# Kernel tuning notes

Hardware: AMD Instinct MI355X
Metric: run time of the kernel (lower is better)

Reference implementation:

```python
import jax, jax.numpy as jnp
import numpy as np

B, M, K = 8, 2048, 64          # clouds, points per cloud, max neighbors
C_IN, C_OUT, R = 64, 64, 0.2   # channels, radius
BN_EPS = 1e-5                  # BatchNorm eval: running_mean=0, running_var=1


def _bn(y, g, b):
    # eval-mode BatchNorm1d with running stats (0, 1)
    return g * y * (1.0 / jnp.sqrt(1.0 + BN_EPS)) + b


def _lin_init(key, fan_in, shape):
    s = 1.0 / np.sqrt(fan_in)
    return jax.random.uniform(key, shape, jnp.float32, -s, s)


def setup_inputs() -> dict:
    key = jax.random.key(0)
    ks = jax.random.split(key, 16)
    N = B * M
    pos = jax.random.uniform(ks[0], (N, 3), jnp.float32)
    x = jax.random.normal(ks[1], (N, C_IN), jnp.float32)
    nrm = jax.random.normal(ks[2], (N, 3), jnp.float32)
    normal = nrm / jnp.linalg.norm(nrm, axis=-1, keepdims=True)
    batch = jnp.repeat(jnp.arange(B, dtype=jnp.int32), M)
    return {
        "x": x, "pos": pos, "normal": normal, "batch": batch,
        # PointTransformerConv linear layers (value / key / query)
        "lin_w": _lin_init(ks[3], C_IN, (C_IN, C_OUT)),
        "lin_b": _lin_init(ks[4], C_IN, (C_OUT,)),
        "lin_src_w": _lin_init(ks[5], C_IN, (C_IN, C_OUT)),
        "lin_src_b": _lin_init(ks[6], C_IN, (C_OUT,)),
        "lin_dst_w": _lin_init(ks[7], C_IN, (C_IN, C_OUT)),
        "lin_dst_b": _lin_init(ks[8], C_IN, (C_OUT,)),
        # pos_nn = MLP([6, C_OUT]): Linear -> BN -> ReLU (Dropout off in eval)
        "pos_w": _lin_init(ks[9], 6, (6, C_OUT)),
        "pos_b": _lin_init(ks[10], 6, (C_OUT,)),
        "pos_g": jnp.ones((C_OUT,), jnp.float32),
        "pos_bt": jnp.zeros((C_OUT,), jnp.float32),
        # attn_nn = MLP([C_OUT, C_OUT])
        "attn_w": _lin_init(ks[11], C_OUT, (C_OUT, C_OUT)),
        "attn_b": _lin_init(ks[12], C_OUT, (C_OUT,)),
        "attn_g": jnp.ones((C_OUT,), jnp.float32),
        "attn_bt": jnp.zeros((C_OUT,), jnp.float32),
    }


def _forward(x, pos, normal, lin_w, lin_b, lin_src_w, lin_src_b,
             lin_dst_w, lin_dst_b, pos_w, pos_b, pos_g, pos_bt,
             attn_w, attn_b, attn_g, attn_bt):
    xb = x.reshape(B, M, C_IN)
    pb = pos.reshape(B, M, 3)
    nb = normal.reshape(B, M, 3)

    # radius(pos, pos, r, batch, batch, max_num_neighbors=K):
    # per-cloud pairwise sq-distances -> K nearest, masked to d <= r.
    d2 = jnp.sum((pb[:, :, None, :] - pb[:, None, :, :]) ** 2, axis=-1)  # [B,M,M]
    neg_d2, idx = jax.lax.top_k(-d2, K)                                   # [B,M,K]
    mask = (-neg_d2) <= R * R                                             # self always valid

    gather = jax.vmap(lambda a, i: a[i])  # per-cloud gather: [M,C],[M,K] -> [M,K,C]

    v = xb @ lin_w + lin_b          # value   [B,M,C]
    kf = xb @ lin_src_w + lin_src_b # key     [B,M,C]
    q = xb @ lin_dst_w + lin_dst_b  # query   [B,M,C]

    vj = gather(v, idx)             # [B,M,K,C]
    kj = gather(kf, idx)
    pj = gather(pb, idx)            # [B,M,K,3]
    nj = gather(nb, idx)

    rel = jnp.concatenate([pb[:, :, None, :] - pj,
                           nb[:, :, None, :] - nj], axis=-1)  # [B,M,K,6]
    delta = jax.nn.relu(_bn(rel @ pos_w + pos_b, pos_g, pos_bt))  # [B,M,K,C]

    alpha = jax.nn.relu(_bn((q[:, :, None, :] - kj + delta) @ attn_w + attn_b,
                            attn_g, attn_bt))                     # [B,M,K,C]
    alpha = jnp.where(mask[..., None], alpha, -jnp.inf)
    w = jax.nn.softmax(alpha, axis=2)                              # softmax over neighbors

    out = jnp.sum(w * (vj + delta), axis=2)                        # [B,M,C]
    return out.reshape(B * M, C_OUT)


def reference(x, pos, normal, batch, lin_w, lin_b, lin_src_w, lin_src_b,
              lin_dst_w, lin_dst_b, pos_w, pos_b, pos_g, pos_bt,
              attn_w, attn_b, attn_g, attn_bt):
    del batch  # batch ids are block-contiguous: encoded by the [B,M] reshape
    return _forward(x, pos, normal, lin_w, lin_b, lin_src_w, lin_src_b,
                    lin_dst_w, lin_dst_b, pos_w, pos_b, pos_g, pos_bt,
                    attn_w, attn_b, attn_g, attn_bt)
```

## Files before the change

kernel.cpp:

```cpp
#include <hip/hip_runtime.h>
#include <math.h>

#define BB 8
#define MM 2048
#define NTOT (BB*MM)
#define R2 0.04f
#define CAP 256

typedef _Float16 h8 __attribute__((ext_vector_type(8)));
typedef _Float16 h4 __attribute__((ext_vector_type(4)));
typedef float f32x4 __attribute__((ext_vector_type(4)));

__device__ __forceinline__ int swz(int row, int col) {
  return (row << 6) + ((((col >> 3) ^ (row & 7)) << 3) | (col & 7));
}

__device__ __forceinline__ unsigned long long shfl_xor_u64(unsigned long long x, int off) {
  int lo = __shfl_xor((int)(unsigned)(x & 0xFFFFFFFFull), off, 64);
  int hi = __shfl_xor((int)(unsigned)(x >> 32), off, 64);
  return (((unsigned long long)(unsigned)hi) << 32) | (unsigned)lo;
}
__device__ __forceinline__ unsigned long long wave_min_u64(unsigned long long x) {
#pragma unroll
  for (int off = 32; off; off >>= 1) {
    unsigned long long o = shfl_xor_u64(x, off);
    x = (o < x) ? o : x;
  }
  return x;
}
__device__ __forceinline__ unsigned long long wave_max_u64(unsigned long long x) {
#pragma unroll
  for (int off = 32; off; off >>= 1) {
    unsigned long long o = shfl_xor_u64(x, off);
    x = (o > x) ? o : x;
  }
  return x;
}

__global__ __launch_bounds__(256) void prep_w(
    const float* __restrict__ attn_w, const float* __restrict__ pos_w,
    const float* __restrict__ lin_w, const float* __restrict__ lsw, const float* __restrict__ ldw,
    const float* __restrict__ lsb, const float* __restrict__ ldb,
    const float* __restrict__ pos_b, const float* __restrict__ pos_g, const float* __restrict__ pos_bt,
    const float* __restrict__ attn_b, const float* __restrict__ attn_g, const float* __restrict__ attn_bt,
    unsigned short* __restrict__ w_img, unsigned short* __restrict__ pw_img,
    unsigned short* __restrict__ pj_img, float* __restrict__ bnc) {
  __shared__ float sWa[4096];
  __shared__ float sK[256], sQ[256];
  const int tid = threadIdx.x, blk = blockIdx.x;
  for (int i = tid; i < 4096; i += 256) sWa[i] = attn_w[i];
  {
    const int r = tid >> 6, c = tid & 63;
    sK[tid] = lsw[(blk * 4 + r) * 64 + c];
    sQ[tid] = ldw[(blk * 4 + r) * 64 + c];
  }
  __syncthreads();
  const int idx = blk * 256 + tid;
  const int d = idx >> 6, cc = idx & 63;
  const int lr = tid >> 6;
  float wka_v = 0.f, wqa_v = 0.f;
  for (int m = 0; m < 64; ++m) {
    const float wac = sWa[m * 64 + cc];
    wka_v = fmaf(sK[lr * 64 + m], wac, wka_v);
    wqa_v = fmaf(sQ[lr * 64 + m], wac, wqa_v);
  }
  const int sp = swz(cc, d);
  w_img[sp] = __builtin_bit_cast(unsigned short, (_Float16)sWa[d * 64 + cc]);
  const float v0 = lin_w[idx];
  const _Float16 h0 = (_Float16)v0;
  pj_img[sp] = __builtin_bit_cast(unsigned short, h0);
  pj_img[4096 + sp] = __builtin_bit_cast(unsigned short, (_Float16)(v0 - (float)h0));
  const _Float16 h1 = (_Float16)wka_v;
  pj_img[8192 + sp] = __builtin_bit_cast(unsigned short, h1);
  pj_img[12288 + sp] = __builtin_bit_cast(unsigned short, (_Float16)(wka_v - (float)h1));
  const _Float16 h2 = (_Float16)wqa_v;
  pj_img[16384 + sp] = __builtin_bit_cast(unsigned short, h2);
  pj_img[20480 + sp] = __builtin_bit_cast(unsigned short, (_Float16)(wqa_v - (float)h2));
  if (idx < 64 * 24) {
    const int col = idx / 24, k = idx - col * 24;
    const float v = (k < 6) ? pos_w[k * 64 + col] : 0.f;
    pw_img[idx] = __builtin_bit_cast(unsigned short, (_Float16)v);
  }
  if (blk == 0 && tid < 64) {
    float bk = 0.f, bq = 0.f;
    for (int m = 0; m < 64; ++m) {
      const float wac = sWa[m * 64 + tid];
      bk = fmaf(lsb[m], wac, bk);
      bq = fmaf(ldb[m], wac, bq);
    }
    const float bninv = 1.0f / sqrtf(1.0f + 1e-5f);
    const float pA = pos_g[tid] * bninv;
    bnc[tid] = pA;
    bnc[64 + tid] = pA * pos_b[tid] + pos_bt[tid];
    const float aA = attn_g[tid] * bninv;
    bnc[128 + tid] = aA;
    bnc[192 + tid] = aA * (attn_b[tid] + bq - bk) + attn_bt[tid];
  }
}

__device__ __forceinline__ void proj_body(
    const float* __restrict__ x, const unsigned short* __restrict__ pj_img,
    const float* __restrict__ b0, float* __restrict__ kv2, float* __restrict__ qwr,
    unsigned short* s_xh, unsigned short* s_xl, int bid) {
  const int tid = threadIdx.x;
  const int r0 = bid << 6;
  {
    const int row = tid >> 2, seg = tid & 3;
    const float* xr = x + (((size_t)(r0 + row)) << 6) + (seg << 4);
    float xb[16];
#pragma unroll
    for (int q = 0; q < 4; ++q) *(float4*)&xb[q * 4] = ((const float4*)xr)[q];
    h8 c0h, c1h, c0l, c1l;
#pragma unroll
    for (int e = 0; e < 8; ++e) {
      const _Float16 h0 = (_Float16)xb[e];
      c0h[e] = h0; c0l[e] = (_Float16)(xb[e] - (float)h0);
      const _Float16 h1 = (_Float16)xb[e + 8];
      c1h[e] = h1; c1l[e] = (_Float16)(xb[e + 8] - (float)h1);
    }
    const int base = row << 6;
    const int oi0 = base + ((((seg << 1) | 0) ^ (row & 7)) << 3);
    const int oi1 = base + ((((seg << 1) | 1) ^ (row & 7)) << 3);
    *(h8*)&s_xh[oi0] = c0h; *(h8*)&s_xh[oi1] = c1h;
    *(h8*)&s_xl[oi0] = c0l; *(h8*)&s_xl[oi1] = c1l;
  }
  __syncthreads();
  const int wv = tid >> 6, lane = tid & 63, lrow = lane >> 4, lcol = lane & 15;
  const int col = (wv << 4) + lcol;
  f32x4 acc[3][4];
#pragma unroll
  for (int o = 0; o < 3; ++o)
#pragma unroll
    for (int mt = 0; mt < 4; ++mt) acc[o][mt] = (f32x4){0.f, 0.f, 0.f, 0.f};
#pragma unroll
  for (int ks = 0; ks < 2; ++ks) {
    const int kc = lrow + (ks << 2);
    const int boff = (col << 6) + ((kc ^ (col & 7)) << 3);
    const h8 bh0 = *(const h8*)&pj_img[boff];
    const h8 bl0 = *(const h8*)&pj_img[4096 + boff];
    const h8 bh1 = *(const h8*)&pj_img[8192 + boff];
    const h8 bl1 = *(const h8*)&pj_img[12288 + boff];
    const h8 bh2 = *(const h8*)&pj_img[16384 + boff];
    const h8 bl2 = *(const h8*)&pj_img[20480 + boff];
#pragma unroll
    for (int mt = 0; mt < 4; ++mt) {
      const int m = (mt << 4) + lcol;
      const int aoff = (m << 6) + ((kc ^ (m & 7)) << 3);
      const h8 ah = *(const h8*)&s_xh[aoff];
      const h8 al = *(const h8*)&s_xl[aoff];
      acc[0][mt] = __builtin_amdgcn_mfma_f32_16x16x32_f16(ah, bh0, acc[0][mt], 0, 0, 0);
      acc[0][mt] = __builtin_amdgcn_mfma_f32_16x16x32_f16(al, bh0, acc[0][mt], 0, 0, 0);
      acc[0][mt] = __builtin_amdgcn_mfma_f32_16x16x32_f16(ah, bl0, acc[0][mt], 0, 0, 0);
      acc[1][mt] = __builtin_amdgcn_mfma_f32_16x16x32_f16(ah, bh1, acc[1][mt], 0, 0, 0);
      acc[1][mt] = __builtin_amdgcn_mfma_f32_16x16x32_f16(al, bh1, acc[1][mt], 0, 0, 0);
      acc[1][mt] = __builtin_amdgcn_mfma_f32_16x16x32_f16(ah, bl1, acc[1][mt], 0, 0, 0);
      acc[2][mt] = __builtin_amdgcn_mfma_f32_16x16x32_f16(ah, bh2, acc[2][mt], 0, 0, 0);
      acc[2][mt] = __builtin_amdgcn_mfma_f32_16x16x32_f16(al, bh2, acc[2][mt], 0, 0, 0);
      acc[2][mt] = __builtin_amdgcn_mfma_f32_16x16x32_f16(ah, bl2, acc[2][mt], 0, 0, 0);
    }
  }
  const float bb0 = b0[col];
#pragma unroll
  for (int mt = 0; mt < 4; ++mt)
#pragma unroll
    for (int r = 0; r < 4; ++r) {
      const size_t row = (size_t)(r0 + (mt << 4) + (lrow << 2) + r);
      *(float2*)&kv2[(row << 7) + (col << 1)] =
          make_float2(acc[1][mt][r], acc[0][mt][r] + bb0);
      qwr[(row << 6) + col] = acc[2][mt][r];
    }
}

__device__ __forceinline__ void knn_body(
    const float* __restrict__ pos, unsigned* __restrict__ nbr,
    float* spos, unsigned long long* slistb, int bid) {
  const int b = bid >> 9;
  const int qblk = bid & 511;
  const int tid = threadIdx.x;
  const float* pc = pos + (size_t)b * MM * 3;
  for (int i = tid; i < MM * 3 / 4; i += 256)
    ((float4*)spos)[i] = ((const float4*)pc)[i];
  __syncthreads();
  const int wv = tid >> 6, lane = tid & 63;
  unsigned long long* slist = slistb + wv * CAP;
  const int q = (qblk << 2) + wv;
  const float qx = spos[q * 3 + 0], qy = spos[q * 3 + 1], qz = spos[q * 3 + 2];
  unsigned bits[32];
  unsigned cnt = 0;
#pragma unroll
  for (int i = 0; i < 32; ++i) {
    const int j = lane + (i << 6);
    const float dx = qx - spos[j * 3 + 0];
    const float dy = qy - spos[j * 3 + 1];
    const float dz = qz - spos[j * 3 + 2];
    const float d2 = __fadd_rn(__fadd_rn(__fmul_rn(dx, dx), __fmul_rn(dy, dy)), __fmul_rn(dz, dz));
    const unsigned bt = __float_as_uint(d2);
    bits[i] = bt;
    const bool val = (d2 <= R2);
    const unsigned long long mb = __ballot(val);
    if (val) {
      const unsigned off = cnt + (unsigned)__popcll(mb & ((1ull << lane) - 1ull));
      if (off < CAP) slist[off] = (((unsigned long long)bt) << 32) | (unsigned)j;
    }
    cnt += (unsigned)__popcll(mb);
  }
  __syncthreads();
  unsigned outv;
  if (cnt <= 64u) {
    if (lane < (int)cnt) outv = ((unsigned)slist[lane]) | 0x80000000u;
    else                 outv = 0u;
  } else if (cnt <= (unsigned)CAP) {
    unsigned long long s0, s1, s2, s3, t;
    s0 = (lane       < (int)cnt) ? slist[lane      ] : ~0ull;
    s1 = (lane + 64  < (int)cnt) ? slist[lane + 64 ] : ~0ull;
    s2 = (lane + 128 < (int)cnt) ? slist[lane + 128] : ~0ull;
    s3 = (lane + 192 < (int)cnt) ? slist[lane + 192] : ~0ull;
    if (s1 < s0) { t = s0; s0 = s1; s1 = t; }
    if (s3 < s2) { t = s2; s2 = s3; s3 = t; }
    if (s2 < s0) { t = s0; s0 = s2; s2 = t; }
    if (s3 < s1) { t = s1; s1 = s3; s3 = t; }
    if (s2 < s1) { t = s1; s1 = s2; s2 = t; }
    if (cnt <= 128u) {
      const int pops = (int)cnt - 64;
      int rl = (cnt > (unsigned)lane) ? (int)((cnt - (unsigned)lane + 63u) >> 6) : 0;
      if (rl > 4) rl = 4;
      int ti = rl - 1;
      for (int p = 0; p < pops; ++p) {
        const unsigned long long mx =
            (ti == 3) ? s3 : (ti == 2) ? s2 : (ti == 1) ? s1 : (ti == 0) ? s0 : 0ull;
        const unsigned long long g = wave_max_u64(mx);
        if (ti >= 0 && mx == g) ti--;
      }
      const int c = ti + 1;
      const unsigned long long b0 = __ballot(c & 1);
      const unsigned long long b1 = __ballot(c & 2);
      const unsigned long long b2 = __ballot(c & 4);
      const unsigned long long lm = (1ull << lane) - 1ull;
      const int pre = __popcll(b0 & lm) + 2 * __popcll(b1 & lm) + 4 * __popcll(b2 & lm);
      if (c > 0) slist[pre + 0] = s0;
      if (c > 1) slist[pre + 1] = s1;
      if (c > 2) slist[pre + 2] = s2;
      if (c > 3) slist[pre + 3] = s3;
      __asm volatile("s_waitcnt lgkmcnt(0)" ::: "memory");
      outv = ((unsigned)slist[lane]) | 0x80000000u;
    } else {
      unsigned long long my = 0;
      for (int it = 0; it < 64; ++it) {
        const unsigned long long gg = wave_min_u64(s0);
        if (lane == it) my = gg;
        if (s0 == gg) { s0 = s1; s1 = s2; s2 = s3; s3 = ~0ull; }
      }
      outv = ((unsigned)my) | 0x80000000u;
    }
  } else {
    unsigned long long cur = ~0ull;
#pragma unroll
    for (int i = 0; i < 32; ++i) {
      const unsigned long long k = (((unsigned long long)bits[i]) << 32) | (unsigned)(lane + (i << 6));
      cur = (k < cur) ? k : cur;
    }
    unsigned long long my = 0;
    for (int it = 0; it < 64; ++it) {
      const unsigned long long gg = wave_min_u64(cur);
      if (lane == it) my = gg;
      if (cur == gg) {
        cur = ~0ull;
#pragma unroll
        for (int i = 0; i < 32; ++i) {
          const unsigned long long k = (((unsigned long long)bits[i]) << 32) | (unsigned)(lane + (i << 6));
          if (k > gg && k < cur) cur = k;
        }
      }
    }
    const float d2s = __uint_as_float((unsigned)(my >> 32));
    outv = ((unsigned)my) | ((d2s <= R2) ? 0x80000000u : 0u);
  }
  nbr[((size_t)(b * MM + q)) * 64 + lane] = outv;
}

__global__ __launch_bounds__(256, 2) void proj_knn(
    const float* __restrict__ x, const unsigned short* __restrict__ pj_img,
    const float* __restrict__ b0, float* __restrict__ kv2, float* __restrict__ qwr,
    const float* __restrict__ pos, unsigned* __restrict__ nbr) {
  __shared__ __align__(16) unsigned char smem[32768];
  if (blockIdx.x < NTOT / 64) {
    proj_body(x, pj_img, b0, kv2, qwr,
              (unsigned short*)smem, (unsigned short*)(smem + 8192), blockIdx.x);
  } else {
    knn_body(pos, nbr, (float*)smem,
             (unsigned long long*)(smem + 24576), blockIdx.x - NTOT / 64);
  }
}

__global__ __launch_bounds__(256, 4) void ptc_kernel(
    const float* __restrict__ pos, const float* __restrict__ nrm,
    const float* __restrict__ kv2, const float* __restrict__ qwr,
    const unsigned* __restrict__ nbr,
    const unsigned short* __restrict__ w_img, const unsigned short* __restrict__ pw_img,
    const float* __restrict__ bnc,
    float* __restrict__ out) {
  __shared__ __align__(16) unsigned short s_t[4096];
  __shared__ __align__(16) unsigned short s_relh[64 * 24];
  const int qi = blockIdx.x;
  const int b = qi >> 11;
  const int tid = threadIdx.x;
  const int wv = tid >> 6, lane = tid & 63;
  const int lrow = lane >> 4, lcol = lane & 15;
  const int col = (wv << 4) + lcol;

  const h8 bh0 = *(const h8*)&w_img[(col << 6) + ((lrow ^ (col & 7)) << 3)];
  const h8 bh1 = *(const h8*)&w_img[(col << 6) + (((lrow + 4) ^ (col & 7)) << 3)];
  const h4 bpw = *(const h4*)&pw_img[col * 24 + (lrow << 2)];
  const float pA = bnc[col], pB = bnc[64 + col];
  const float aA = bnc[128 + col];
  const float qwc = qwr[(size_t)qi * 64 + col];
  const float aBq = fmaf(aA, qwc, bnc[192 + col]);

  uint4 sraw[4];
#pragma unroll
  for (int mt = 0; mt < 4; ++mt)
    sraw[mt] = *(const uint4*)&nbr[(size_t)qi * 64 + (mt << 4) + (lrow << 2)];
  float kwv[16], vvv[16];
  unsigned mbits = 0;
#pragma unroll
  for (int mt = 0; mt < 4; ++mt) {
    const unsigned sv[4] = {sraw[mt].x, sraw[mt].y, sraw[mt].z, sraw[mt].w};
#pragma unroll
    for (int r = 0; r < 4; ++r) {
      const int i = (mt << 2) + r;
      const unsigned s = sv[r];
      mbits |= ((s >> 31) & 1u) << i;
      const size_t jg = ((size_t)(b << 11) + (size_t)(s & 0x7FFFFFFFu));
      const float2 kv = *(const float2*)&kv2[(jg << 7) + (col << 1)];
      kwv[i] = kv.x;
      vvv[i] = kv.y;
    }
  }

  if (tid < 64) {
    const unsigned s = nbr[(size_t)qi * 64 + tid];
    const int jg = (b << 11) + (int)(s & 0x7FFFFFFFu);
    h8 hv;
    hv[0] = (_Float16)(pos[(size_t)qi * 3 + 0] - pos[(size_t)jg * 3 + 0]);
    hv[1] = (_Float16)(pos[(size_t)qi * 3 + 1] - pos[(size_t)jg * 3 + 1]);
    hv[2] = (_Float16)(pos[(size_t)qi * 3 + 2] - pos[(size_t)jg * 3 + 2]);
    hv[3] = (_Float16)(nrm[(size_t)qi * 3 + 0] - nrm[(size_t)jg * 3 + 0]);
    hv[4] = (_Float16)(nrm[(size_t)qi * 3 + 1] - nrm[(size_t)jg * 3 + 1]);
    hv[5] = (_Float16)(nrm[(size_t)qi * 3 + 2] - nrm[(size_t)jg * 3 + 2]);
    hv[6] = (_Float16)0.f; hv[7] = (_Float16)0.f;
    *(h8*)&s_relh[tid * 24] = hv;
    h8 zz = (h8)(_Float16)0.f;
    *(h8*)&s_relh[tid * 24 + 8] = zz;
  }
  __syncthreads();

  f32x4 dacc[4];
#pragma unroll
  for (int mt = 0; mt < 4; ++mt) {
    const h4 ar = *(const h4*)&s_relh[((mt << 4) + lcol) * 24 + (lrow << 2)];
    dacc[mt] = __builtin_amdgcn_mfma_f32_16x16x16f16(ar, bpw, (f32x4){0.f, 0.f, 0.f, 0.f}, 0, 0, 0);
  }

  float def[16];
#pragma unroll
  for (int mt = 0; mt < 4; ++mt) {
#pragma unroll
    for (int r = 0; r < 4; ++r) {
      const int i = (mt << 2) + r;
      const int n = (mt << 4) + (lrow << 2) + r;
      const float de = fmaxf(fmaf(pA, dacc[mt][r], pB), 0.f);
      def[i] = de;
      *(_Float16*)&s_t[swz(n, col)] = (_Float16)de;
    }
  }
  __syncthreads();

  f32x4 acc[4];
#pragma unroll
  for (int mt = 0; mt < 4; ++mt) acc[mt] = (f32x4){0.f, 0.f, 0.f, 0.f};
#pragma unroll
  for (int mt = 0; mt < 4; ++mt) {
    const int m = (mt << 4) + lcol;
    const h8 ah0 = *(const h8*)&s_t[(m << 6) + ((lrow ^ (m & 7)) << 3)];
    acc[mt] = __builtin_amdgcn_mfma_f32_16x16x32_f16(ah0, bh0, acc[mt], 0, 0, 0);
    const h8 ah1 = *(const h8*)&s_t[(m << 6) + (((lrow + 4) ^ (m & 7)) << 3)];
    acc[mt] = __builtin_amdgcn_mfma_f32_16x16x32_f16(ah1, bh1, acc[mt], 0, 0, 0);
  }

  float ps = 0.f;
#pragma unroll
  for (int mt = 0; mt < 4; ++mt) {
#pragma unroll
    for (int r = 0; r < 4; ++r) {
      const int i = (mt << 2) + r;
      const float al = fmaxf(fmaf(aA, acc[mt][r] - kwv[i], aBq), 0.f);
      const float e = ((mbits >> i) & 1u) ? __expf(al) : 0.f;
      kwv[i] = e;
      ps += e;
    }
  }
  ps += __shfl_xor(ps, 16, 64);
  ps += __shfl_xor(ps, 32, 64);

  float o = 0.f;
#pragma unroll
  for (int i = 0; i < 16; ++i) o = fmaf(kwv[i], vvv[i] + def[i], o);
  o += __shfl_xor(o, 16, 64);
  o += __shfl_xor(o, 32, 64);
  if (lrow == 0) out[(size_t)qi * 64 + col] = o * (1.0f / ps);
}

extern "C" void kernel_launch(void* const* d_in, const int* in_sizes, int n_in,
                              void* d_out, int out_size, void* d_ws, size_t ws_size,
                              hipStream_t stream) {
  const float* x      = (const float*)d_in[0];
  const float* pos    = (const float*)d_in[1];
  const float* nrm    = (const float*)d_in[2];
  const float* lin_w  = (const float*)d_in[4];
  const float* lin_b  = (const float*)d_in[5];
  const float* lsw    = (const float*)d_in[6];
  const float* lsb    = (const float*)d_in[7];
  const float* ldw    = (const float*)d_in[8];
  const float* ldb    = (const float*)d_in[9];
  const float* pos_w  = (const float*)d_in[10];
  const float* pos_b  = (const float*)d_in[11];
  const float* pos_g  = (const float*)d_in[12];
  const float* pos_bt = (const float*)d_in[13];
  const float* attn_w = (const float*)d_in[14];
  const float* attn_b = (const float*)d_in[15];
  const float* attn_g = (const float*)d_in[16];
  const float* attn_bt= (const float*)d_in[17];
  float* out = (float*)d_out;

  float* wsf = (float*)d_ws;
  float* kv2  = wsf;
  float* qwr  = wsf + (size_t)NTOT * 128;
  unsigned* nbr = (unsigned*)(wsf + (size_t)NTOT * 192);
  unsigned short* w_img  = (unsigned short*)(wsf + (size_t)NTOT * 192 + (size_t)NTOT * 64);
  unsigned short* pw_img = w_img + 4096;
  unsigned short* pj_img = pw_img + 1536;
  float* bnc  = (float*)(pj_img + 24576);

  prep_w<<<16, 256, 0, stream>>>(attn_w, pos_w, lin_w, lsw, ldw, lsb, ldb,
                                 pos_b, pos_g, pos_bt, attn_b, attn_g, attn_bt,
                                 w_img, pw_img, pj_img, bnc);
  proj_knn<<<NTOT / 64 + BB * (MM / 4), 256, 0, stream>>>(
      x, pj_img, lin_b, kv2, qwr, pos, nbr);
  ptc_kernel<<<NTOT, 256, 0, stream>>>(
      pos, nrm, kv2, qwr, nbr, w_img, pw_img, bnc, out);
}
```

Before: 122.1 us.

## Process four queries per wave in kNN blocks and schedule kNN before projection

Each kNN block now handles 16 queries (four per wave, in a loop) instead of four, so the per-cloud position staging into shared memory is amortised over four times as many queries and the block count drops from 4096 to 1024. The bits[32] register array is removed, and the rare over-capacity fallback recomputes distances on each selection pass, which lowers register pressure. kNN blocks are placed ahead of projection blocks in the fused launch so the longer kNN work starts first. The cost is less parallelism per block and serial loops over queries and distance chunks (unroll 1), which could lengthen the critical path.

```diff
diff --git a/kernel.cpp b/kernel.cpp
--- a/kernel.cpp
+++ b/kernel.cpp
@@ -6,6 +6,7 @@
 #define NTOT (BB*MM)
 #define R2 0.04f
 #define CAP 256
+#define KNNB 1024
 
 typedef _Float16 h8 __attribute__((ext_vector_type(8)));
 typedef _Float16 h4 __attribute__((ext_vector_type(4)));
@@ -171,11 +172,11 @@
     }
 }
 
-__device__ __forceinline__ void knn_body(
+__device__ __forceinline__ void knn_body16(
     const float* __restrict__ pos, unsigned* __restrict__ nbr,
     float* spos, unsigned long long* slistb, int bid) {
-  const int b = bid >> 9;
-  const int qblk = bid & 511;
+  const int b = bid >> 7;
+  const int q16 = bid & 127;
   const int tid = threadIdx.x;
   const float* pc = pos + (size_t)b * MM * 3;
   for (int i = tid; i < MM * 3 / 4; i += 256)
@@ -183,99 +184,97 @@
   __syncthreads();
   const int wv = tid >> 6, lane = tid & 63;
   unsigned long long* slist = slistb + wv * CAP;
-  const int q = (qblk << 2) + wv;
-  const float qx = spos[q * 3 + 0], qy = spos[q * 3 + 1], qz = spos[q * 3 + 2];
-  unsigned bits[32];
-  unsigned cnt = 0;
-#pragma unroll
-  for (int i = 0; i < 32; ++i) {
-    const int j = lane + (i << 6);
-    const float dx = qx - spos[j * 3 + 0];
-    const float dy = qy - spos[j * 3 + 1];
-    const float dz = qz - spos[j * 3 + 2];
-    const float d2 = __fadd_rn(__fadd_rn(__fmul_rn(dx, dx), __fmul_rn(dy, dy)), __fmul_rn(dz, dz));
-    const unsigned bt = __float_as_uint(d2);
-    bits[i] = bt;
-    const bool val = (d2 <= R2);
-    const unsigned long long mb = __ballot(val);
-    if (val) {
-      const unsigned off = cnt + (unsigned)__popcll(mb & ((1ull << lane) - 1ull));
-      if (off < CAP) slist[off] = (((unsigned long long)bt) << 32) | (unsigned)j;
-    }
-    cnt += (unsigned)__popcll(mb);
-  }
-  __syncthreads();
-  unsigned outv;
-  if (cnt <= 64u) {
-    if (lane < (int)cnt) outv = ((unsigned)slist[lane]) | 0x80000000u;
-    else                 outv = 0u;
-  } else if (cnt <= (unsigned)CAP) {
-    unsigned long long s0, s1, s2, s3, t;
-    s0 = (lane       < (int)cnt) ? slist[lane      ] : ~0ull;
-    s1 = (lane + 64  < (int)cnt) ? slist[lane + 64 ] : ~0ull;
-    s2 = (lane + 128 < (int)cnt) ? slist[lane + 128] : ~0ull;
-    s3 = (lane + 192 < (int)cnt) ? slist[lane + 192] : ~0ull;
-    if (s1 < s0) { t = s0; s0 = s1; s1 = t; }
-    if (s3 < s2) { t = s2; s2 = s3; s3 = t; }
-    if (s2 < s0) { t = s0; s0 = s2; s2 = t; }
-    if (s3 < s1) { t = s1; s1 = s3; s3 = t; }
-    if (s2 < s1) { t = s1; s1 = s2; s2 = t; }
-    if (cnt <= 128u) {
-      const int pops = (int)cnt - 64;
-      int rl = (cnt > (unsigned)lane) ? (int)((cnt - (unsigned)lane + 63u) >> 6) : 0;
-      if (rl > 4) rl = 4;
-      int ti = rl - 1;
-      for (int p = 0; p < pops; ++p) {
-        const unsigned long long mx =
-            (ti == 3) ? s3 : (ti == 2) ? s2 : (ti == 1) ? s1 : (ti == 0) ? s0 : 0ull;
-        const unsigned long long g = wave_max_u64(mx);
-        if (ti >= 0 && mx == g) ti--;
+#pragma unroll 1
+  for (int qq = 0; qq < 4; ++qq) {
+    const int q = (q16 << 4) + (wv << 2) + qq;
+    const float qx = spos[q * 3 + 0], qy = spos[q * 3 + 1], qz = spos[q * 3 + 2];
+    unsigned cnt = 0;
+#pragma unroll 1
+    for (int i = 0; i < 32; ++i) {
+      const int j = lane + (i << 6);
+      const float dx = qx - spos[j * 3 + 0];
+      const float dy = qy - spos[j * 3 + 1];
+      const float dz = qz - spos[j * 3 + 2];
+      const float d2 = __fadd_rn(__fadd_rn(__fmul_rn(dx, dx), __fmul_rn(dy, dy)), __fmul_rn(dz, dz));
+      const bool val = (d2 <= R2);
+      const unsigned long long mb = __ballot(val);
+      if (val) {
+        const unsigned off = cnt + (unsigned)__popcll(mb & ((1ull << lane) - 1ull));
+        if (off < CAP) slist[off] = (((unsigned long long)__float_as_uint(d2)) << 32) | (unsigned)j;
       }
-      const int c = ti + 1;
-      const unsigned long long b0 = __ballot(c & 1);
-      const unsigned long long b1 = __ballot(c & 2);
-      const unsigned long long b2 = __ballot(c & 4);
-      const unsigned long long lm = (1ull << lane) - 1ull;
-      const int pre = __popcll(b0 & lm) + 2 * __popcll(b1 & lm) + 4 * __popcll(b2 & lm);
-      if (c > 0) slist[pre + 0] = s0;
-      if (c > 1) slist[pre + 1] = s1;
-      if (c > 2) slist[pre + 2] = s2;
-      if (c > 3) slist[pre + 3] = s3;
-      __asm volatile("s_waitcnt lgkmcnt(0)" ::: "memory");
-      outv = ((unsigned)slist[lane]) | 0x80000000u;
+      cnt += (unsigned)__popcll(mb);
+    }
+    __asm volatile("s_waitcnt lgkmcnt(0)" ::: "memory");
+    unsigned outv;
+    if (cnt <= 64u) {
+      if (lane < (int)cnt) outv = ((unsigned)slist[lane]) | 0x80000000u;
+      else                 outv = 0u;
+    } else if (cnt <= (unsigned)CAP) {
+      unsigned long long s0, s1, s2, s3, t;
+      s0 = (lane       < (int)cnt) ? slist[lane      ] : ~0ull;
+      s1 = (lane + 64  < (int)cnt) ? slist[lane + 64 ] : ~0ull;
+      s2 = (lane + 128 < (int)cnt) ? slist[lane + 128] : ~0ull;
+      s3 = (lane + 192 < (int)cnt) ? slist[lane + 192] : ~0ull;
+      if (s1 < s0) { t = s0; s0 = s1; s1 = t; }
+      if (s3 < s2) { t = s2; s2 = s3; s3 = t; }
+      if (s2 < s0) { t = s0; s0 = s2; s2 = t; }
+      if (s3 < s1) { t = s1; s1 = s3; s3 = t; }
+      if (s2 < s1) { t = s1; s1 = s2; s2 = t; }
+      if (cnt <= 128u) {
+        const int pops = (int)cnt - 64;
+        int rl = (cnt > (unsigned)lane) ? (int)((cnt - (unsigned)lane + 63u) >> 6) : 0;
+        if (rl > 4) rl = 4;
+        int ti = rl - 1;
+        for (int p = 0; p < pops; ++p) {
+          const unsigned long long mx =
+              (ti == 3) ? s3 : (ti == 2) ? s2 : (ti == 1) ? s1 : (ti == 0) ? s0 : 0ull;
+          const unsigned long long g = wave_max_u64(mx);
+          if (ti >= 0 && mx == g) ti--;
+        }
+        const int c = ti + 1;
+        const unsigned long long b0 = __ballot(c & 1);
+        const unsigned long long b1 = __ballot(c & 2);
+        const unsigned long long b2 = __ballot(c & 4);
+        const unsigned long long lm = (1ull << lane) - 1ull;
+        const int pre = __popcll(b0 & lm) + 2 * __popcll(b1 & lm) + 4 * __popcll(b2 & lm);
+        if (c > 0) slist[pre + 0] = s0;
+        if (c > 1) slist[pre + 1] = s1;
+        if (c > 2) slist[pre + 2] = s2;
+        if (c > 3) slist[pre + 3] = s3;
+        __asm volatile("s_waitcnt lgkmcnt(0)" ::: "memory");
+        outv = ((unsigned)slist[lane]) | 0x80000000u;
+      } else {
+        unsigned long long my = 0;
+        for (int it = 0; it < 64; ++it) {
+          const unsigned long long gg = wave_min_u64(s0);
+          if (lane == it) my = gg;
+          if (s0 == gg) { s0 = s1; s1 = s2; s2 = s3; s3 = ~0ull; }
+        }
+        outv = ((unsigned)my) | 0x80000000u;
+      }
     } else {
+      unsigned long long prev = 0;
       unsigned long long my = 0;
       for (int it = 0; it < 64; ++it) {
-        const unsigned long long gg = wave_min_u64(s0);
+        unsigned long long cur = ~0ull;
+        for (int i = 0; i < 32; ++i) {
+          const int j = lane + (i << 6);
+          const float dx = qx - spos[j * 3 + 0];
+          const float dy = qy - spos[j * 3 + 1];
+          const float dz = qz - spos[j * 3 + 2];
+          const float d2 = __fadd_rn(__fadd_rn(__fmul_rn(dx, dx), __fmul_rn(dy, dy)), __fmul_rn(dz, dz));
+          const unsigned long long k = (((unsigned long long)__float_as_uint(d2)) << 32) | (unsigned)j;
+          if (k > prev && k < cur) cur = k;
+        }
+        const unsigned long long gg = wave_min_u64(cur);
         if (lane == it) my = gg;
-        if (s0 == gg) { s0 = s1; s1 = s2; s2 = s3; s3 = ~0ull; }
+        prev = gg;
       }
-      outv = ((unsigned)my) | 0x80000000u;
-    }
-  } else {
-    unsigned long long cur = ~0ull;
-#pragma unroll
-    for (int i = 0; i < 32; ++i) {
-      const unsigned long long k = (((unsigned long long)bits[i]) << 32) | (unsigned)(lane + (i << 6));
-      cur = (k < cur) ? k : cur;
-    }
-    unsigned long long my = 0;
-    for (int it = 0; it < 64; ++it) {
-      const unsigned long long gg = wave_min_u64(cur);
-      if (lane == it) my = gg;
-      if (cur == gg) {
-        cur = ~0ull;
-#pragma unroll
-        for (int i = 0; i < 32; ++i) {
-          const unsigned long long k = (((unsigned long long)bits[i]) << 32) | (unsigned)(lane + (i << 6));
-          if (k > gg && k < cur) cur = k;
-        }
-      }
-    }
-    const float d2s = __uint_as_float((unsigned)(my >> 32));
-    outv = ((unsigned)my) | ((d2s <= R2) ? 0x80000000u : 0u);
-  }
-  nbr[((size_t)(b * MM + q)) * 64 + lane] = outv;
+      const float d2s = __uint_as_float((unsigned)(my >> 32));
+      outv = ((unsigned)my) | ((d2s <= R2) ? 0x80000000u : 0u);
+    }
+    nbr[((size_t)(b * MM + q)) * 64 + lane] = outv;
+  }
 }
 
 __global__ __launch_bounds__(256, 2) void proj_knn(
@@ -283,12 +282,12 @@
     const float* __restrict__ b0, float* __restrict__ kv2, float* __restrict__ qwr,
     const float* __restrict__ pos, unsigned* __restrict__ nbr) {
   __shared__ __align__(16) unsigned char smem[32768];
-  if (blockIdx.x < NTOT / 64) {
+  if (blockIdx.x < KNNB) {
+    knn_body16(pos, nbr, (float*)smem,
+               (unsigned long long*)(smem + 24576), blockIdx.x);
+  } else {
     proj_body(x, pj_img, b0, kv2, qwr,
-              (unsigned short*)smem, (unsigned short*)(smem + 8192), blockIdx.x);
-  } else {
-    knn_body(pos, nbr, (float*)smem,
-             (unsigned long long*)(smem + 24576), blockIdx.x - NTOT / 64);
+              (unsigned short*)smem, (unsigned short*)(smem + 8192), blockIdx.x - KNNB);
   }
 }
 
@@ -444,7 +443,7 @@
   prep_w<<<16, 256, 0, stream>>>(attn_w, pos_w, lin_w, lsw, ldw, lsb, ldb,
                                  pos_b, pos_g, pos_bt, attn_b, attn_g, attn_bt,
                                  w_img, pw_img, pj_img, bnc);
-  proj_knn<<<NTOT / 64 + BB * (MM / 4), 256, 0, stream>>>(
+  proj_knn<<<KNNB + NTOT / 64, 256, 0, stream>>>(
       x, pj_img, lin_b, kv2, qwr, pos, nbr);
   ptc_kernel<<<NTOT, 256, 0, stream>>>(
       pos, nrm, kv2, qwr, nbr, w_img, pw_img, bnc, out);
```

Result: no change. 119.9 us (-1.8%).
